# Kernel tuning notes

Measured on AMD Instinct MI355X. Metric: run time of the kernel, lower is better.

## Reference

```python
import jax, jax.numpy as jnp
import numpy as np

N = 131072          # total rows across all types
IN_C = 512          # in_channels
OUT_C = 512         # out_channels
NUM_TYPES = 8       # len(types)


def setup_inputs() -> dict:
    key = jax.random.key(0)
    k1, k2, k3, k4 = jax.random.split(key, 4)
    x = jax.random.normal(k1, (N, IN_C), dtype=jnp.float32)
    type_vec = jnp.sort(jax.random.randint(k2, (N,), 0, NUM_TYPES)).astype(jnp.int64)
    # HeteroLinear params: weight [num_types, in, out], bias [num_types, out]
    scale = 1.0 / np.sqrt(IN_C)
    weight = jax.random.normal(k3, (NUM_TYPES, IN_C, OUT_C), dtype=jnp.float32) * scale
    bias = jax.random.normal(k4, (NUM_TYPES, OUT_C), dtype=jnp.float32) * scale
    return {"x": x, "type_vec": type_vec, "weight": weight, "bias": bias}


def _grouped_linear(x, type_vec, weight, bias):
    """out[n] = x[n] @ weight[type_vec[n]] + bias[type_vec[n]].

    Computed as T masked dense GEMMs (T is small) to avoid gathering a
    [N, in, out] per-row weight tensor.
    """
    n, out_c = x.shape[0], weight.shape[2]

    def per_type(acc, t):
        mask = (type_vec == t).astype(x.dtype)[:, None]  # [N, 1]
        y = (x * mask) @ weight[t] + mask * bias[t]      # [N, out]
        return acc + y, None

    out, _ = jax.lax.scan(per_type,
                          jnp.zeros((n, out_c), dtype=x.dtype),
                          jnp.arange(weight.shape[0]))
    return out


def reference(x, type_vec, weight, bias):
    # Equivalent to ToHeteroLinear.fused_forward (and dict_forward after the
    # cat/repeat_interleave, since type_vec is sorted / is_sorted=True).
    return _grouped_linear(x, type_vec, weight, bias)
```

## Files before the change

kernel.cpp:

```cpp
#include <hip/hip_runtime.h>

#define NROWS 131072
#define KDIM 512
#define NDIM 512

using short8  = __attribute__((ext_vector_type(8))) short;
using float4v = __attribute__((ext_vector_type(4))) float;
using uint4v  = __attribute__((ext_vector_type(4))) unsigned int;

__device__ __forceinline__ unsigned pack_trunc(float a, float b) {
    unsigned ua = __builtin_bit_cast(unsigned, a);
    unsigned ub = __builtin_bit_cast(unsigned, b);
    return __builtin_amdgcn_perm(ub, ua, 0x07060302u);
}
__device__ __forceinline__ unsigned pack_round(float a, float b) {
    unsigned ua = __builtin_bit_cast(unsigned, a) + 0x8000u;
    unsigned ub = __builtin_bit_cast(unsigned, b) + 0x8000u;
    return __builtin_amdgcn_perm(ub, ua, 0x07060302u);
}

__global__ __launch_bounds__(256) void wconv_kernel(const float* __restrict__ w,
                                                    unsigned short* __restrict__ wt) {
    int b  = blockIdx.x;
    int ty = b >> 6;
    int ot = (b >> 3) & 7;
    int it = b & 7;
    __shared__ float tile[64][65];
    const float* wp = w + ((size_t)ty << 18);
    int tid = threadIdx.x;
    int cf = tid & 15, ir0 = tid >> 4;
    #pragma unroll
    for (int j = 0; j < 4; ++j) {
        int ir = ir0 + 16 * j;
        float4v v = *(const float4v*)(wp + (size_t)(it * 64 + ir) * NDIM + ot * 64 + cf * 4);
        tile[ir][cf * 4 + 0] = v.x;
        tile[ir][cf * 4 + 1] = v.y;
        tile[ir][cf * 4 + 2] = v.z;
        tile[ir][cf * 4 + 3] = v.w;
    }
    __syncthreads();
    int oc = tid >> 2, iq = tid & 3;
    unsigned* op = (unsigned*)(wt + ((size_t)ty << 18) + (size_t)(ot * 64 + oc) * KDIM + it * 64 + iq * 16);
    #pragma unroll
    for (int j = 0; j < 8; ++j)
        op[j] = pack_round(tile[iq * 16 + 2 * j][oc], tile[iq * 16 + 2 * j + 1][oc]);
}

__global__ __launch_bounds__(256, 2)
void hetero_gemm_kernel(const float* __restrict__ x,
                        const int* __restrict__ tv,
                        const unsigned short* __restrict__ wt,
                        const float* __restrict__ bias,
                        float* __restrict__ out) {
    __shared__ uint4v ldsA[4 * 128];
    __shared__ uint4v ldsB[4 * 128];

    const int b = blockIdx.x;
    const int rowTile = ((b >> 5) << 3) | (b & 7);
    const int colTile = (b >> 3) & 3;
    const int row0 = rowTile << 7;
    const int col0 = colTile << 7;

    const int tid  = threadIdx.x;
    const int lane = tid & 63;
    const int wave = tid >> 6;
    const int wm   = (wave & 1) << 6;
    const int wn   = (wave >> 1) << 6;
    const int l15  = lane & 15;
    const int quad = lane >> 4;

    const int ra = tid >> 1;
    const int khalf = tid & 1;
    const int rtypeA = tv[row0 + ra];

    const int nb = tid & 127;
    const int g2 = tid >> 7;

    const int t0 = tv[row0];
    const int t1 = tv[row0 + 127];

    float4v acc[4][4];
    float4v zero = {0.f, 0.f, 0.f, 0.f};
    #pragma unroll
    for (int i = 0; i < 4; ++i)
        #pragma unroll
        for (int j = 0; j < 4; ++j)
            acc[i][j] = zero;

    for (int tt = t0; tt <= t1; ++tt) {
        const unsigned maskA = (rtypeA == tt) ? 0xFFFFFFFFu : 0u;
        const float* ap = x + (size_t)(row0 + ra) * KDIM + khalf * 16;
        const unsigned short* wb = wt + ((size_t)tt << 18) + (size_t)(col0 + nb) * KDIM;

        float4v av[4];
        uint4v  bv[2];
        #pragma unroll
        for (int i = 0; i < 4; ++i) av[i] = *(const float4v*)(ap + i * 4);
        bv[0] = *(const uint4v*)(wb + g2 * 8);
        bv[1] = *(const uint4v*)(wb + (g2 + 2) * 8);

        for (int kc = 0; kc < KDIM; kc += 32) {
            __syncthreads();
            uint4v pa0, pa1;
            pa0.x = pack_trunc(av[0].x, av[0].y) & maskA;
            pa0.y = pack_trunc(av[0].z, av[0].w) & maskA;
            pa0.z = pack_trunc(av[1].x, av[1].y) & maskA;
            pa0.w = pack_trunc(av[1].z, av[1].w) & maskA;
            pa1.x = pack_trunc(av[2].x, av[2].y) & maskA;
            pa1.y = pack_trunc(av[2].z, av[2].w) & maskA;
            pa1.z = pack_trunc(av[3].x, av[3].y) & maskA;
            pa1.w = pack_trunc(av[3].z, av[3].w) & maskA;
            ldsA[(khalf * 2 + 0) * 128 + ra] = pa0;
            ldsA[(khalf * 2 + 1) * 128 + ra] = pa1;
            ldsB[(g2    ) * 128 + nb] = bv[0];
            ldsB[(g2 + 2) * 128 + nb] = bv[1];
            __syncthreads();

            if (kc + 32 < KDIM) {
                const float* ap2 = ap + kc + 32;
                #pragma unroll
                for (int i = 0; i < 4; ++i) av[i] = *(const float4v*)(ap2 + i * 4);
                const unsigned short* wb2 = wb + kc + 32;
                bv[0] = *(const uint4v*)(wb2 + g2 * 8);
                bv[1] = *(const uint4v*)(wb2 + (g2 + 2) * 8);
            }

            short8 af[4], bf[4];
            #pragma unroll
            for (int mi = 0; mi < 4; ++mi)
                af[mi] = *(const short8*)&ldsA[quad * 128 + wm + mi * 16 + l15];
            #pragma unroll
            for (int ni = 0; ni < 4; ++ni)
                bf[ni] = *(const short8*)&ldsB[quad * 128 + wn + ni * 16 + l15];
            #pragma unroll
            for (int mi = 0; mi < 4; ++mi)
                #pragma unroll
                for (int ni = 0; ni < 4; ++ni)
                    acc[mi][ni] = __builtin_amdgcn_mfma_f32_16x16x32_bf16(
                        af[mi], bf[ni], acc[mi][ni], 0, 0, 0);
        }
    }

    #pragma unroll
    for (int mi = 0; mi < 4; ++mi) {
        #pragma unroll
        for (int r = 0; r < 4; ++r) {
            const int grow = row0 + wm + mi * 16 + quad * 4 + r;
            const int rt = tv[grow];
            const float* brow = bias + (size_t)rt * NDIM;
            float* orow = out + (size_t)grow * NDIM;
            #pragma unroll
            for (int ni = 0; ni < 4; ++ni) {
                const int gcol = col0 + wn + ni * 16 + l15;
                orow[gcol] = acc[mi][ni][r] + brow[gcol];
            }
        }
    }
}

extern "C" void kernel_launch(void* const* d_in, const int* in_sizes, int n_in,
                              void* d_out, int out_size, void* d_ws, size_t ws_size,
                              hipStream_t stream) {
    const float* x    = (const float*)d_in[0];
    const int*   tv   = (const int*)d_in[1];
    const float* w    = (const float*)d_in[2];
    const float* bias = (const float*)d_in[3];
    float* out = (float*)d_out;
    unsigned short* wtr = (unsigned short*)d_ws;

    wconv_kernel<<<512, 256, 0, stream>>>(w, wtr);
    hetero_gemm_kernel<<<4096, 256, 0, stream>>>(x, tv, wtr, bias, out);
}
```

Measured before the change: 549.7 us.

## Double-buffer LDS with direct global-to-LDS weight loads and per-type masked epilogue

Weight tiles now go straight from global memory into LDS through global_load_lds into a double buffer. The A-tile pack-and-store is moved after the MFMAs so the next tile is staged while the current one is computed, which leaves one barrier per k-step instead of two. Input masking is dropped; instead each type gets its own accumulator pass, and only rows of that type are written in the epilogue, using nontemporal stores. Occupancy is raised to 4 blocks per CU, which may increase register pressure, and boundary tiles now store the output once per type.

```diff
diff --git a/kernel.cpp b/kernel.cpp
--- a/kernel.cpp
+++ b/kernel.cpp
@@ -17,6 +17,12 @@
     unsigned ua = __builtin_bit_cast(unsigned, a) + 0x8000u;
     unsigned ub = __builtin_bit_cast(unsigned, b) + 0x8000u;
     return __builtin_amdgcn_perm(ub, ua, 0x07060302u);
+}
+
+__device__ __forceinline__ void glds16(const void* g, void* l) {
+    __builtin_amdgcn_global_load_lds(
+        (__attribute__((address_space(1))) void*)g,
+        (__attribute__((address_space(3))) void*)l, 16, 0, 0);
 }
 
 __global__ __launch_bounds__(256) void wconv_kernel(const float* __restrict__ w,
@@ -46,14 +52,14 @@
         op[j] = pack_round(tile[iq * 16 + 2 * j][oc], tile[iq * 16 + 2 * j + 1][oc]);
 }
 
-__global__ __launch_bounds__(256, 2)
+__global__ __launch_bounds__(256, 4)
 void hetero_gemm_kernel(const float* __restrict__ x,
                         const int* __restrict__ tv,
                         const unsigned short* __restrict__ wt,
                         const float* __restrict__ bias,
                         float* __restrict__ out) {
-    __shared__ uint4v ldsA[4 * 128];
-    __shared__ uint4v ldsB[4 * 128];
+    __shared__ uint4v ldsA[2][4 * 128];
+    __shared__ uint4v ldsB[2][4 * 128];
 
     const int b = blockIdx.x;
     const int rowTile = ((b >> 5) << 3) | (b & 7);
@@ -69,9 +75,8 @@
     const int l15  = lane & 15;
     const int quad = lane >> 4;
 
-    const int ra = tid >> 1;
+    const int ra    = tid >> 1;
     const int khalf = tid & 1;
-    const int rtypeA = tv[row0 + ra];
 
     const int nb = tid & 127;
     const int g2 = tid >> 7;
@@ -79,80 +84,100 @@
     const int t0 = tv[row0];
     const int t1 = tv[row0 + 127];
 
-    float4v acc[4][4];
-    float4v zero = {0.f, 0.f, 0.f, 0.f};
-    #pragma unroll
-    for (int i = 0; i < 4; ++i)
-        #pragma unroll
-        for (int j = 0; j < 4; ++j)
-            acc[i][j] = zero;
+    const float* apBase = x + (size_t)(row0 + ra) * KDIM + khalf * 16;
 
     for (int tt = t0; tt <= t1; ++tt) {
-        const unsigned maskA = (rtypeA == tt) ? 0xFFFFFFFFu : 0u;
-        const float* ap = x + (size_t)(row0 + ra) * KDIM + khalf * 16;
-        const unsigned short* wb = wt + ((size_t)tt << 18) + (size_t)(col0 + nb) * KDIM;
+        const unsigned short* wbase =
+            wt + ((size_t)tt << 18) + (size_t)(col0 + nb) * KDIM + g2 * 8;
+
+        float4v acc[4][4];
+        float4v zero = {0.f, 0.f, 0.f, 0.f};
+        #pragma unroll
+        for (int i = 0; i < 4; ++i)
+            #pragma unroll
+            for (int j = 0; j < 4; ++j)
+                acc[i][j] = zero;
 
         float4v av[4];
-        uint4v  bv[2];
         #pragma unroll
-        for (int i = 0; i < 4; ++i) av[i] = *(const float4v*)(ap + i * 4);
-        bv[0] = *(const uint4v*)(wb + g2 * 8);
-        bv[1] = *(const uint4v*)(wb + (g2 + 2) * 8);
+        for (int i = 0; i < 4; ++i) av[i] = *(const float4v*)(apBase + i * 4);
+        glds16(wbase,      &ldsB[0][ g2      * 128 + nb]);
+        glds16(wbase + 16, &ldsB[0][(g2 + 2) * 128 + nb]);
+        {
+            uint4v pa0, pa1;
+            pa0.x = pack_trunc(av[0].x, av[0].y);
+            pa0.y = pack_trunc(av[0].z, av[0].w);
+            pa0.z = pack_trunc(av[1].x, av[1].y);
+            pa0.w = pack_trunc(av[1].z, av[1].w);
+            pa1.x = pack_trunc(av[2].x, av[2].y);
+            pa1.y = pack_trunc(av[2].z, av[2].w);
+            pa1.z = pack_trunc(av[3].x, av[3].y);
+            pa1.w = pack_trunc(av[3].z, av[3].w);
+            ldsA[0][(khalf * 2 + 0) * 128 + ra] = pa0;
+            ldsA[0][(khalf * 2 + 1) * 128 + ra] = pa1;
+        }
+        __syncthreads();
 
+        int cur = 0;
         for (int kc = 0; kc < KDIM; kc += 32) {
-            __syncthreads();
-            uint4v pa0, pa1;
-            pa0.x = pack_trunc(av[0].x, av[0].y) & maskA;
-            pa0.y = pack_trunc(av[0].z, av[0].w) & maskA;
-            pa0.z = pack_trunc(av[1].x, av[1].y) & maskA;
-            pa0.w = pack_trunc(av[1].z, av[1].w) & maskA;
-            pa1.x = pack_trunc(av[2].x, av[2].y) & maskA;
-            pa1.y = pack_trunc(av[2].z, av[2].w) & maskA;
-            pa1.z = pack_trunc(av[3].x, av[3].y) & maskA;
-            pa1.w = pack_trunc(av[3].z, av[3].w) & maskA;
-            ldsA[(khalf * 2 + 0) * 128 + ra] = pa0;
-            ldsA[(khalf * 2 + 1) * 128 + ra] = pa1;
-            ldsB[(g2    ) * 128 + nb] = bv[0];
-            ldsB[(g2 + 2) * 128 + nb] = bv[1];
-            __syncthreads();
-
             if (kc + 32 < KDIM) {
-                const float* ap2 = ap + kc + 32;
+                const float* ap2 = apBase + kc + 32;
                 #pragma unroll
                 for (int i = 0; i < 4; ++i) av[i] = *(const float4v*)(ap2 + i * 4);
-                const unsigned short* wb2 = wb + kc + 32;
-                bv[0] = *(const uint4v*)(wb2 + g2 * 8);
-                bv[1] = *(const uint4v*)(wb2 + (g2 + 2) * 8);
+                glds16(wbase + kc + 32,      &ldsB[cur ^ 1][ g2      * 128 + nb]);
+                glds16(wbase + kc + 32 + 16, &ldsB[cur ^ 1][(g2 + 2) * 128 + nb]);
             }
 
             short8 af[4], bf[4];
             #pragma unroll
             for (int mi = 0; mi < 4; ++mi)
-                af[mi] = *(const short8*)&ldsA[quad * 128 + wm + mi * 16 + l15];
+                af[mi] = *(const short8*)&ldsA[cur][quad * 128 + wm + mi * 16 + l15];
             #pragma unroll
             for (int ni = 0; ni < 4; ++ni)
-                bf[ni] = *(const short8*)&ldsB[quad * 128 + wn + ni * 16 + l15];
+                bf[ni] = *(const short8*)&ldsB[cur][quad * 128 + wn + ni * 16 + l15];
+
             #pragma unroll
             for (int mi = 0; mi < 4; ++mi)
                 #pragma unroll
                 for (int ni = 0; ni < 4; ++ni)
                     acc[mi][ni] = __builtin_amdgcn_mfma_f32_16x16x32_bf16(
                         af[mi], bf[ni], acc[mi][ni], 0, 0, 0);
+
+            if (kc + 32 < KDIM) {
+                uint4v pa0, pa1;
+                pa0.x = pack_trunc(av[0].x, av[0].y);
+                pa0.y = pack_trunc(av[0].z, av[0].w);
+                pa0.z = pack_trunc(av[1].x, av[1].y);
+                pa0.w = pack_trunc(av[1].z, av[1].w);
+                pa1.x = pack_trunc(av[2].x, av[2].y);
+                pa1.y = pack_trunc(av[2].z, av[2].w);
+                pa1.z = pack_trunc(av[3].x, av[3].y);
+                pa1.w = pack_trunc(av[3].z, av[3].w);
+                ldsA[cur ^ 1][(khalf * 2 + 0) * 128 + ra] = pa0;
+                ldsA[cur ^ 1][(khalf * 2 + 1) * 128 + ra] = pa1;
+            }
+            __syncthreads();
+            cur ^= 1;
         }
-    }
 
-    #pragma unroll
-    for (int mi = 0; mi < 4; ++mi) {
+        float bcol[4];
         #pragma unroll
-        for (int r = 0; r < 4; ++r) {
-            const int grow = row0 + wm + mi * 16 + quad * 4 + r;
-            const int rt = tv[grow];
-            const float* brow = bias + (size_t)rt * NDIM;
-            float* orow = out + (size_t)grow * NDIM;
+        for (int ni = 0; ni < 4; ++ni)
+            bcol[ni] = bias[(size_t)tt * NDIM + col0 + wn + ni * 16 + l15];
+
+        #pragma unroll
+        for (int mi = 0; mi < 4; ++mi) {
             #pragma unroll
-            for (int ni = 0; ni < 4; ++ni) {
-                const int gcol = col0 + wn + ni * 16 + l15;
-                orow[gcol] = acc[mi][ni][r] + brow[gcol];
+            for (int r = 0; r < 4; ++r) {
+                const int grow = row0 + wm + mi * 16 + quad * 4 + r;
+                if (tv[grow] == tt) {
+                    float* orow = out + (size_t)grow * NDIM;
+                    #pragma unroll
+                    for (int ni = 0; ni < 4; ++ni) {
+                        const int gcol = col0 + wn + ni * 16 + l15;
+                        __builtin_nontemporal_store(acc[mi][ni][r] + bcol[ni], &orow[gcol]);
+                    }
+                }
             }
         }
     }
```

Result: slower. 795.4 us (+44.7%).

## Pre-convert x to bf16 and stream tiles via global_load_lds double buffering

Applied to the files above, without the earlier changes.

Adds a separate kernel that converts x to bf16 in workspace, then a new GEMM kernel that loads A and B tiles directly into double-buffered LDS with global_load_lds. Each type in a row tile gets its own accumulators, and only the rows of that type are written. This replaces the old approach of masking A for every type. The change aims to halve A-read traffic in the GEMM, remove register-staged conversion, and overlap loads with MFMA, at the cost of an extra pass over x (read 256MB fp32, write 128MB bf16) and a workspace-size dependency. The old kernel stays as a fallback when workspace is too small.

```diff
diff --git a/kernel.cpp b/kernel.cpp
--- a/kernel.cpp
+++ b/kernel.cpp
@@ -17,6 +17,12 @@
     unsigned ua = __builtin_bit_cast(unsigned, a) + 0x8000u;
     unsigned ub = __builtin_bit_cast(unsigned, b) + 0x8000u;
     return __builtin_amdgcn_perm(ub, ua, 0x07060302u);
+}
+
+__device__ __forceinline__ void glds16(const void* g, void* l) {
+    __builtin_amdgcn_global_load_lds(
+        (__attribute__((address_space(1))) void*)g,
+        (__attribute__((address_space(3))) void*)l, 16, 0, 0);
 }
 
 __global__ __launch_bounds__(256) void wconv_kernel(const float* __restrict__ w,
@@ -46,12 +52,131 @@
         op[j] = pack_round(tile[iq * 16 + 2 * j][oc], tile[iq * 16 + 2 * j + 1][oc]);
 }
 
+__global__ __launch_bounds__(256) void xconv_kernel(const float* __restrict__ x,
+                                                    unsigned short* __restrict__ xb) {
+    const size_t total = (size_t)NROWS * KDIM / 8;
+    size_t i = (size_t)blockIdx.x * 256 + threadIdx.x;
+    const size_t stride = (size_t)gridDim.x * 256;
+    const float4v* xv = (const float4v*)x;
+    uint4v* ov = (uint4v*)xb;
+    for (; i < total; i += stride) {
+        float4v a = __builtin_nontemporal_load(&xv[2 * i]);
+        float4v c = __builtin_nontemporal_load(&xv[2 * i + 1]);
+        uint4v o;
+        o.x = pack_round(a.x, a.y);
+        o.y = pack_round(a.z, a.w);
+        o.z = pack_round(c.x, c.y);
+        o.w = pack_round(c.z, c.w);
+        ov[i] = o;
+    }
+}
+
+__global__ __launch_bounds__(256, 3)
+void hetero_gemm_pre(const unsigned short* __restrict__ xb,
+                     const int* __restrict__ tv,
+                     const unsigned short* __restrict__ wt,
+                     const float* __restrict__ bias,
+                     float* __restrict__ out) {
+    __shared__ uint4v ldsA[2][4 * 128];
+    __shared__ uint4v ldsB[2][4 * 128];
+
+    const int b = blockIdx.x;
+    const int rowTile = ((b >> 5) << 3) | (b & 7);
+    const int colTile = (b >> 3) & 3;
+    const int row0 = rowTile << 7;
+    const int col0 = colTile << 7;
+
+    const int tid  = threadIdx.x;
+    const int lane = tid & 63;
+    const int wave = tid >> 6;
+    const int wm   = (wave & 1) << 6;
+    const int wn   = (wave >> 1) << 6;
+    const int l15  = lane & 15;
+    const int quad = lane >> 4;
+
+    const int i128 = tid & 127;
+    const int g2   = tid >> 7;
+
+    const int t0 = tv[row0];
+    const int t1 = tv[row0 + 127];
+
+    const unsigned short* abase = xb + (size_t)(row0 + i128) * KDIM + g2 * 8;
+
+    for (int tt = t0; tt <= t1; ++tt) {
+        const unsigned short* wbase =
+            wt + ((size_t)tt << 18) + (size_t)(col0 + i128) * KDIM + g2 * 8;
+
+        float4v acc[4][4];
+        float4v zero = {0.f, 0.f, 0.f, 0.f};
+        #pragma unroll
+        for (int i = 0; i < 4; ++i)
+            #pragma unroll
+            for (int j = 0; j < 4; ++j)
+                acc[i][j] = zero;
+
+        glds16(abase,      &ldsA[0][ g2      * 128 + i128]);
+        glds16(abase + 16, &ldsA[0][(g2 + 2) * 128 + i128]);
+        glds16(wbase,      &ldsB[0][ g2      * 128 + i128]);
+        glds16(wbase + 16, &ldsB[0][(g2 + 2) * 128 + i128]);
+        __syncthreads();
+
+        int cur = 0;
+        for (int kc = 0; kc < KDIM; kc += 32) {
+            if (kc + 32 < KDIM) {
+                glds16(abase + kc + 32,      &ldsA[cur ^ 1][ g2      * 128 + i128]);
+                glds16(abase + kc + 48,      &ldsA[cur ^ 1][(g2 + 2) * 128 + i128]);
+                glds16(wbase + kc + 32,      &ldsB[cur ^ 1][ g2      * 128 + i128]);
+                glds16(wbase + kc + 48,      &ldsB[cur ^ 1][(g2 + 2) * 128 + i128]);
+            }
+
+            short8 af[4], bf[4];
+            #pragma unroll
+            for (int mi = 0; mi < 4; ++mi)
+                af[mi] = *(const short8*)&ldsA[cur][quad * 128 + wm + mi * 16 + l15];
+            #pragma unroll
+            for (int ni = 0; ni < 4; ++ni)
+                bf[ni] = *(const short8*)&ldsB[cur][quad * 128 + wn + ni * 16 + l15];
+
+            #pragma unroll
+            for (int mi = 0; mi < 4; ++mi)
+                #pragma unroll
+                for (int ni = 0; ni < 4; ++ni)
+                    acc[mi][ni] = __builtin_amdgcn_mfma_f32_16x16x32_bf16(
+                        af[mi], bf[ni], acc[mi][ni], 0, 0, 0);
+
+            __syncthreads();
+            cur ^= 1;
+        }
+
+        float bcol[4];
+        #pragma unroll
+        for (int ni = 0; ni < 4; ++ni)
+            bcol[ni] = bias[(size_t)tt * NDIM + col0 + wn + ni * 16 + l15];
+
+        #pragma unroll
+        for (int mi = 0; mi < 4; ++mi) {
+            #pragma unroll
+            for (int r = 0; r < 4; ++r) {
+                const int grow = row0 + wm + mi * 16 + quad * 4 + r;
+                if (tv[grow] == tt) {
+                    float* orow = out + (size_t)grow * NDIM;
+                    #pragma unroll
+                    for (int ni = 0; ni < 4; ++ni) {
+                        const int gcol = col0 + wn + ni * 16 + l15;
+                        __builtin_nontemporal_store(acc[mi][ni][r] + bcol[ni], &orow[gcol]);
+                    }
+                }
+            }
+        }
+    }
+}
+
 __global__ __launch_bounds__(256, 2)
-void hetero_gemm_kernel(const float* __restrict__ x,
-                        const int* __restrict__ tv,
-                        const unsigned short* __restrict__ wt,
-                        const float* __restrict__ bias,
-                        float* __restrict__ out) {
+void hetero_gemm_fallback(const float* __restrict__ x,
+                          const int* __restrict__ tv,
+                          const unsigned short* __restrict__ wt,
+                          const float* __restrict__ bias,
+                          float* __restrict__ out) {
     __shared__ uint4v ldsA[4 * 128];
     __shared__ uint4v ldsB[4 * 128];
 
@@ -166,8 +291,17 @@
     const float* w    = (const float*)d_in[2];
     const float* bias = (const float*)d_in[3];
     float* out = (float*)d_out;
+
     unsigned short* wtr = (unsigned short*)d_ws;
+    const size_t WTN  = (size_t)8 * 512 * 512;
+    const size_t NEED = WTN * 2 + (size_t)NROWS * KDIM * 2;
 
     wconv_kernel<<<512, 256, 0, stream>>>(w, wtr);
-    hetero_gemm_kernel<<<4096, 256, 0, stream>>>(x, tv, wtr, bias, out);
-}
+    if (ws_size >= NEED) {
+        unsigned short* xb = wtr + WTN;
+        xconv_kernel<<<2048, 256, 0, stream>>>(x, xb);
+        hetero_gemm_pre<<<4096, 256, 0, stream>>>(xb, tv, wtr, bias, out);
+    } else {
+        hetero_gemm_fallback<<<4096, 256, 0, stream>>>(x, tv, wtr, bias, out);
+    }
+}
```

New measurement: 671.1 us. 22.1% more time.
